# Performance work log

Hardware: AMD Instinct MI355X
Metric: run time of the kernel (lower is better)

The kernel has to match this reference:

```python
import jax, jax.numpy as jnp
import numpy as np

L = 18                      # tree depth, N = 2**L - 1 nodes (complete binary tree)
N = 2**L - 1               # 262143
D = 128                     # embedding dim
V = 100000                  # vocab size of the single data type
E = 8                       # edge_count


def setup_inputs() -> dict:
    key = jax.random.key(0)
    ks = jax.random.split(key, 8)
    data = jax.random.randint(ks[0], (N,), 0, V)
    edges = jax.random.randint(ks[1], (N,), 0, E)
    data_vecs = jax.random.normal(ks[2], (V, D), dtype=jnp.float32) * 0.1
    # torch uses torch.rand (U[0,1)); scaled for numerical stability over 18 levels
    data_W = jax.random.uniform(ks[3], (D, D), dtype=jnp.float32) * 0.1
    data_b = jax.random.uniform(ks[4], (D,), dtype=jnp.float32) * 0.1
    edge_W = jax.random.uniform(ks[5], (E, D, D), dtype=jnp.float32) * (2.0 / D)
    edge_b = jax.random.uniform(ks[6], (E, D), dtype=jnp.float32) * 0.1
    score_W = jax.random.uniform(ks[7], (D, 1), dtype=jnp.float32)
    return {"data": data, "edges": edges, "data_vecs": data_vecs,
            "data_W": data_W, "data_b": data_b, "edge_W": edge_W,
            "edge_b": edge_b, "score_W": score_W}


def reference(data, edges, data_vecs, data_W, data_b, edge_W, edge_b, score_W):
    # per-node leaf term: addmm(data_bias, data_vecs[data], data_W)  -> [N, D]
    raw = data_vecs[data] @ data_W + data_b
    ret = raw    # value returned to the parent (leaves: unclamped)
    emb = raw    # stored embedding (internal nodes: pre-clamp h)
    # bottom-up over levels; level l occupies indices [2**l - 1, 2**(l+1) - 1)
    for l in reversed(range(L - 1)):
        p0, npar = 2**l - 1, 2**l
        c0, M = 2**(l + 1) - 1, 2**(l + 1)
        child_ret = ret[c0:c0 + M]              # [M, D], siblings adjacent
        eids = edges[c0:c0 + M]                 # [M]
        # edge-weighted child transform: child @ edge_W[e] + edge_b[e]
        contrib = edge_b[eids]
        for e in range(E):                      # small static edge loop
            contrib = contrib + jnp.where((eids == e)[:, None], child_ret, 0.0) @ edge_W[e]
        # sum the two children of each parent, then (leaf + children) / (nc + 1)
        contrib = contrib.reshape(npar, 2, D).sum(axis=1)
        h = (raw[p0:p0 + npar] + contrib) / 3.0
        emb = emb.at[p0:p0 + npar].set(h)
        ret = ret.at[p0:p0 + npar].set(jnp.maximum(h, 0.0))
    scores = (emb @ score_W)[:, 0]              # [N]
    return scores


if __name__ == "__main__":
    out = reference(**setup_inputs())
    print(out.shape, out.dtype)
```

## Files before the change

### kernel.cpp

```cpp
#include <hip/hip_runtime.h>

#define D 128
#define NLVL 17
#define TS 128
#define LVLPAD 1024
#define LDSTR 136
#define LEAF_BLKS 1032
#define CHUNK 2048
#define CNT_BLKS 128

typedef float  floatx4 __attribute__((ext_vector_type(4)));
typedef short  shortx8 __attribute__((ext_vector_type(8)));

__device__ __forceinline__ unsigned short f2bf(float f) {
    unsigned u = __float_as_uint(f);
    u += 0x7FFFu + ((u >> 16) & 1u);
    return (unsigned short)(u >> 16);
}
__device__ __forceinline__ float bf2f(unsigned short h) {
    return __uint_as_float(((unsigned)h) << 16);
}
__device__ __forceinline__ int lvl_base_dev(int l) { return ((2 << l) - 2) + LVLPAD * l; }

__global__ __launch_bounds__(256) void prep_kernel(
    const float* __restrict__ dW, const float* __restrict__ db,
    const float* __restrict__ eW, const float* __restrict__ eb,
    const float* __restrict__ sWs, const float* __restrict__ vecs,
    const int* __restrict__ edges,
    unsigned short* __restrict__ ewt, unsigned short* __restrict__ cwt,
    unsigned short* __restrict__ dwt, float* __restrict__ dcomp,
    float* __restrict__ sv, float* __restrict__ s0, int* __restrict__ ctr,
    int* __restrict__ gcnt128, int Nn,
    unsigned short* __restrict__ vbf, int n4)
{
    __shared__ float smem[8448];
    const int b = blockIdx.x, t = threadIdx.x;
    if (b < 32) {
        float* w_s = smem;
        float* cs  = smem + 4096;
        const int e = b >> 2, cc = b & 3;
        for (int i = t; i < D * 8; i += 256) {
            const int k = i >> 3, j4 = i & 7;
            ((float4*)w_s)[i] = ((const float4*)eW)[((size_t)e * D + k) * 32 + cc * 8 + j4];
        }
        __syncthreads();
        const int r2 = t >> 1, h = t & 1;
        float4 acc[4];
        #pragma unroll
        for (int m = 0; m < 4; m++) acc[m] = make_float4(0.f, 0.f, 0.f, 0.f);
        for (int k = 0; k < D; k++) {
            const float a = dW[(size_t)r2 * D + k];
            #pragma unroll
            for (int m = 0; m < 4; m++) {
                const float4 w4 = ((const float4*)w_s)[k * 8 + h * 4 + m];
                acc[m].x += a * w4.x; acc[m].y += a * w4.y; acc[m].z += a * w4.z; acc[m].w += a * w4.w;
            }
        }
        #pragma unroll
        for (int m = 0; m < 4; m++) {
            cs[r2 * 33 + h * 16 + m * 4 + 0] = acc[m].x;
            cs[r2 * 33 + h * 16 + m * 4 + 1] = acc[m].y;
            cs[r2 * 33 + h * 16 + m * 4 + 2] = acc[m].z;
            cs[r2 * 33 + h * 16 + m * 4 + 3] = acc[m].w;
        }
        __syncthreads();
        {
            const int nn = t >> 3, kseg = t & 7, k0 = kseg * 16;
            unsigned ow[8];
            #pragma unroll
            for (int i2 = 0; i2 < 8; i2++) {
                const unsigned short lo = f2bf(cs[(k0 + 2 * i2) * 33 + nn]);
                const unsigned short hi = f2bf(cs[(k0 + 2 * i2 + 1) * 33 + nn]);
                ow[i2] = (unsigned)lo | ((unsigned)hi << 16);
            }
            uint4* dstp = (uint4*)(cwt + (size_t)e * D * D + (size_t)(cc * 32 + nn) * D + k0);
            dstp[0] = make_uint4(ow[0], ow[1], ow[2], ow[3]);
            dstp[1] = make_uint4(ow[4], ow[5], ow[6], ow[7]);
        }
        if (t < 32) {
            float a2 = 0.f;
            for (int k = 0; k < D; k++) a2 += db[k] * w_s[k * 32 + t];
            dcomp[e * D + cc * 32 + t] = a2 + eb[e * D + cc * 32 + t];
        }
    } else if (b < 41) {
        float* lds = smem;
        const int bb = b - 32;
        const float* src = (bb < 8) ? (eW + (size_t)bb * D * D) : dW;
        unsigned short* dst = (bb < 8) ? (ewt + (size_t)bb * D * D) : dwt;
        for (int half = 0; half < 2; half++) {
            __syncthreads();
            for (int i = t; i < 64 * D / 4; i += 256) {
                float4 v = ((const float4*)src)[half * (64 * D / 4) + i];
                const int k = (i * 4) >> 7, n = (i * 4) & 127;
                lds[k * 129 + n]     = v.x;
                lds[k * 129 + n + 1] = v.y;
                lds[k * 129 + n + 2] = v.z;
                lds[k * 129 + n + 3] = v.w;
            }
            __syncthreads();
            const int n = t >> 1, hh = t & 1;
            for (int kk = 0; kk < 32; kk++) {
                const int k = hh * 32 + kk;
                dst[(size_t)n * D + half * 64 + k] = f2bf(lds[k * 129 + n]);
            }
        }
    } else if (b == 41) {
        float* red = smem;
        if (t < 32) ctr[t] = 0;
        if (t < D) {
            float acc = 0.f;
            for (int j = 0; j < D; j++) acc += dW[(size_t)t * D + j] * sWs[j];
            sv[t] = acc;
        }
        red[t] = (t < D) ? db[t] * sWs[t] : 0.f;
        __syncthreads();
        for (int s = 128; s > 0; s >>= 1) { if (t < s) red[t] += red[t + s]; __syncthreads(); }
        if (t == 0) s0[0] = red[0];
    } else if (b < 42 + CNT_BLKS) {
        int* lc = (int*)smem;
        if (t < 32) lc[t] = 0;
        __syncthreads();
        for (int c = 16383 + (b - 42) * 256 + t; c < Nn; c += CNT_BLKS * 256) {
            const int e = edges[c];
            const int p = (c - 1) >> 1;
            const int l = 31 - __clz(p + 1);
            atomicAdd(&lc[(l - 13) * 8 + e], 1);
        }
        __syncthreads();
        if (t < 32) gcnt128[(b - 42) * 32 + t] = lc[t];
    } else {
        for (int i = (b - 42 - CNT_BLKS) * 256 + t; i < n4; i += (gridDim.x - 42 - CNT_BLKS) * 256) {
            const float4 v = ((const float4*)vecs)[i];
            uint2 o;
            o.x = (unsigned)f2bf(v.x) | ((unsigned)f2bf(v.y) << 16);
            o.y = (unsigned)f2bf(v.z) | ((unsigned)f2bf(v.w) << 16);
            ((uint2*)vbf)[i] = o;
        }
    }
}

__global__ __launch_bounds__(256) void place_kernel(
    const int* __restrict__ edges, const int* __restrict__ gcnt128,
    int* __restrict__ gstart, int* __restrict__ glim,
    int* __restrict__ ctr, int* __restrict__ perm, int Nn)
{
    __shared__ unsigned char key_s[CHUNK];
    __shared__ int part[256];
    __shared__ int tot[32];
    __shared__ int lcnt[32], lbase[32];
    __shared__ int gs_s[4 * 9], gl_s[32];
    const int t = threadIdx.x;
    {
        const int k = t & 31, bs = t >> 5;
        int s = 0;
        for (int bb = bs; bb < CNT_BLKS; bb += 8) s += gcnt128[bb * 32 + k];
        part[t] = s;
    }
    if (t < 32) lcnt[t] = 0;
    __syncthreads();
    if (t < 32) {
        int tt = 0;
        #pragma unroll
        for (int i = 0; i < 8; i++) tt += part[t + 32 * i];
        tot[t] = tt;
    }
    __syncthreads();
    if (t == 0) {
        for (int li = 0; li < 4; li++) {
            int acc = 0;
            for (int e = 0; e < 8; e++) {
                gs_s[li * 9 + e] = acc;
                gl_s[li * 8 + e] = acc + tot[li * 8 + e];
                acc = (acc + tot[li * 8 + e] + (TS - 1)) & ~(TS - 1);
            }
            gs_s[li * 9 + 8] = acc;
        }
    }
    __syncthreads();
    if (blockIdx.x == 0 && t < 36) {
        gstart[13 * 9 + t] = gs_s[t];
        if (t < 32) glim[13 * 8 + t] = gl_s[t];
    }
    const int base = 16383 + blockIdx.x * CHUNK;
    for (int i = t; i < CHUNK; i += 256) {
        const int c = base + i;
        if (c < Nn) {
            const int e = edges[c];
            const int p = (c - 1) >> 1;
            const int l = 31 - __clz(p + 1);
            const int kk = (l - 13) * 8 + e;
            key_s[i] = (unsigned char)kk;
            atomicAdd(&lcnt[kk], 1);
        } else key_s[i] = 255;
    }
    __syncthreads();
    if (t < 32) {
        const int n = lcnt[t];
        lbase[t] = n ? atomicAdd(&ctr[t], n) : 0;
        lcnt[t] = 0;
    }
    __syncthreads();
    for (int i = t; i < CHUNK; i += 256) {
        const int c = base + i;
        if (c >= Nn) continue;
        const int kk = key_s[i];
        if (kk == 255) continue;
        const int off = atomicAdd(&lcnt[kk], 1);
        const int l = (kk >> 3) + 13, e = kk & 7;
        const int pos = gs_s[(l - 13) * 9 + e] + lbase[kk] + off;
        perm[lvl_base_dev(l) + pos] = c;
    }
}

__global__ __launch_bounds__(256, 4) void leaf_embed_kernel(
    unsigned short* __restrict__ X,
    const unsigned short* __restrict__ vbf,
    const int* __restrict__ data,
    const int* __restrict__ perm,
    const int* __restrict__ gstart9,
    const int* __restrict__ glim8,
    const unsigned short* __restrict__ cwt,
    const float* __restrict__ dcomp,
    const float* __restrict__ sv, const float* __restrict__ s0p,
    const unsigned short* __restrict__ dwt,
    const float* __restrict__ db,
    float* __restrict__ out,
    int NI, int lbase_leaf)
{
    __shared__ unsigned short a_s[TS * LDSTR];
    const int t = threadIdx.x;
    const bool is_leaf = (blockIdx.x < LEAF_BLKS);
    const int r = t >> 1, h = t & 1;

    int e = 0, c;
    const unsigned short* Wg;
    const float* bias;
    if (is_leaf) {
        const int ts = blockIdx.x * TS;
        if (ts >= gstart9[8]) return;
        #pragma unroll
        for (int j = 1; j < 8; j++) if (ts >= gstart9[j]) e = j;
        const int p = ts + r;
        c = (p < glim8[e]) ? perm[lbase_leaf + p] : -1;
        Wg = cwt + (size_t)e * D * D;
        bias = dcomp + (size_t)e * D;
    } else {
        const int node = (blockIdx.x - LEAF_BLKS) * TS + r;
        c = (node < NI) ? node : -1;
        Wg = dwt;
        bias = db;
    }

    {
        unsigned short* dst = a_s + r * LDSTR + h * 64;
        if (c >= 0) {
            const uint4* src = (const uint4*)(vbf + (size_t)data[c] * D + h * 64);
            if (is_leaf) {
                float sc = 0.f;
                #pragma unroll
                for (int j = 0; j < 8; j++) {
                    const uint4 v = src[j];
                    const unsigned* pv = (const unsigned*)&v;
                    #pragma unroll
                    for (int u = 0; u < 4; u++) {
                        const int n = h * 64 + j * 8 + u * 2;
                        sc += bf2f((unsigned short)pv[u]) * sv[n]
                            + bf2f((unsigned short)(pv[u] >> 16)) * sv[n + 1];
                    }
                    ((uint4*)dst)[j] = v;
                }
                sc += __shfl_xor(sc, 1, 64);
                if (h == 0) out[c] = sc + s0p[0];
            } else {
                #pragma unroll
                for (int j = 0; j < 8; j++) ((uint4*)dst)[j] = src[j];
            }
        } else {
            #pragma unroll
            for (int j = 0; j < 8; j++) ((uint4*)dst)[j] = make_uint4(0u, 0u, 0u, 0u);
        }
    }
    __syncthreads();

    const int lane = t & 63, wv = t >> 6;
    const int cq = lane & 15, q = lane >> 4;
    const floatx4 z4 = {0.f, 0.f, 0.f, 0.f};
    floatx4 acc[8][2];
    #pragma unroll
    for (int i = 0; i < 8; i++) { acc[i][0] = z4; acc[i][1] = z4; }
    #pragma unroll
    for (int ks = 0; ks < 4; ks++) {
        shortx8 bfr[2];
        #pragma unroll
        for (int nl = 0; nl < 2; nl++) {
            const int n = (wv * 2 + nl) * 16 + cq;
            bfr[nl] = *(const shortx8*)(Wg + (size_t)n * D + ks * 32 + q * 8);
        }
        #pragma unroll
        for (int mt = 0; mt < 8; mt++) {
            const shortx8 af = *(const shortx8*)(a_s + (mt * 16 + cq) * LDSTR + ks * 32 + q * 8);
            acc[mt][0] = __builtin_amdgcn_mfma_f32_16x16x32_bf16(af, bfr[0], acc[mt][0], 0, 0, 0);
            acc[mt][1] = __builtin_amdgcn_mfma_f32_16x16x32_bf16(af, bfr[1], acc[mt][1], 0, 0, 0);
        }
    }
    __syncthreads();
    #pragma unroll
    for (int nl = 0; nl < 2; nl++) {
        const int n = (wv * 2 + nl) * 16 + cq;
        const float bn = bias[n];
        #pragma unroll
        for (int mt = 0; mt < 8; mt++) {
            #pragma unroll
            for (int rg = 0; rg < 4; rg++) {
                const int m = mt * 16 + q * 4 + rg;
                a_s[m * LDSTR + n] = f2bf(acc[mt][nl][rg] + bn);
            }
        }
    }
    __syncthreads();
    if (c >= 0) {
        uint4* dst = (uint4*)(X + (size_t)c * D + h * 64);
        const uint4* srcl = (const uint4*)(a_s + r * LDSTR + h * 64);
        #pragma unroll
        for (int j = 0; j < 8; j++) dst[j] = srcl[j];
    }
}

__global__ __launch_bounds__(256, 4) void tree_gemm_kernel(
    unsigned short* __restrict__ X,
    const int* __restrict__ perm,
    const int* __restrict__ gstart9,
    const int* __restrict__ glim8,
    const unsigned short* __restrict__ ewt,
    const float* __restrict__ eb,
    const float* __restrict__ svec,
    float* __restrict__ out,
    int lbase)
{
    __shared__ unsigned short a_s[TS * LDSTR];
    const int t = threadIdx.x;
    const int ts = blockIdx.x * TS;
    if (ts >= gstart9[8]) return;
    int e = 0;
    #pragma unroll
    for (int j = 1; j < 8; j++) if (ts >= gstart9[j]) e = j;
    const int r = t >> 1, h = t & 1;
    const int p = ts + r;
    const int c = (p < glim8[e]) ? perm[lbase + p] : -1;
    const unsigned short* Wg = ewt + (size_t)e * D * D;

    {
        unsigned short* dst = a_s + r * LDSTR + h * 64;
        if (c >= 0) {
            const uint4* xr = (const uint4*)(X + (size_t)c * D + h * 64);
            const uint4* ya = (const uint4*)(X + (size_t)(2 * c + 1) * D + h * 64);
            const uint4* yb = (const uint4*)(X + (size_t)(2 * c + 2) * D + h * 64);
            const float inv3 = 1.0f / 3.0f;
            float sc = 0.f;
            #pragma unroll
            for (int j = 0; j < 8; j++) {
                uint4 ra = xr[j], rb = ya[j], rc = yb[j];
                const unsigned* pa = (const unsigned*)&ra;
                const unsigned* pb = (const unsigned*)&rb;
                const unsigned* pc = (const unsigned*)&rc;
                unsigned ou[4];
                #pragma unroll
                for (int u = 0; u < 4; u++) {
                    const float h0 = (bf2f((unsigned short)pa[u]) + bf2f((unsigned short)pb[u])
                                    + bf2f((unsigned short)pc[u])) * inv3;
                    const float h1 = (bf2f((unsigned short)(pa[u] >> 16)) + bf2f((unsigned short)(pb[u] >> 16))
                                    + bf2f((unsigned short)(pc[u] >> 16))) * inv3;
                    const int n = h * 64 + j * 8 + u * 2;
                    sc += h0 * svec[n] + h1 * svec[n + 1];
                    unsigned short q0 = f2bf(h0), q1 = f2bf(h1);
                    q0 = (q0 & 0x8000u) ? 0 : q0;
                    q1 = (q1 & 0x8000u) ? 0 : q1;
                    ou[u] = (unsigned)q0 | ((unsigned)q1 << 16);
                }
                ((uint4*)dst)[j] = make_uint4(ou[0], ou[1], ou[2], ou[3]);
            }
            sc += __shfl_xor(sc, 1, 64);
            if (h == 0) out[c] = sc;
        } else {
            #pragma unroll
            for (int j = 0; j < 8; j++) ((uint4*)dst)[j] = make_uint4(0u, 0u, 0u, 0u);
        }
    }
    __syncthreads();
    const int lane = t & 63, wv = t >> 6;
    const int cq = lane & 15, q = lane >> 4;
    const floatx4 z4 = {0.f, 0.f, 0.f, 0.f};
    floatx4 acc[8][2];
    #pragma unroll
    for (int i = 0; i < 8; i++) { acc[i][0] = z4; acc[i][1] = z4; }
    #pragma unroll
    for (int ks = 0; ks < 4; ks++) {
        shortx8 bfr[2];
        #pragma unroll
        for (int nl = 0; nl < 2; nl++) {
            const int n = (wv * 2 + nl) * 16 + cq;
            bfr[nl] = *(const shortx8*)(Wg + (size_t)n * D + ks * 32 + q * 8);
        }
        #pragma unroll
        for (int mt = 0; mt < 8; mt++) {
            const shortx8 af = *(const shortx8*)(a_s + (mt * 16 + cq) * LDSTR + ks * 32 + q * 8);
            acc[mt][0] = __builtin_amdgcn_mfma_f32_16x16x32_bf16(af, bfr[0], acc[mt][0], 0, 0, 0);
            acc[mt][1] = __builtin_amdgcn_mfma_f32_16x16x32_bf16(af, bfr[1], acc[mt][1], 0, 0, 0);
        }
    }
    __syncthreads();
    #pragma unroll
    for (int nl = 0; nl < 2; nl++) {
        const int n = (wv * 2 + nl) * 16 + cq;
        const float bn = eb[(size_t)e * D + n];
        #pragma unroll
        for (int mt = 0; mt < 8; mt++) {
            #pragma unroll
            for (int rg = 0; rg < 4; rg++) {
                const int m = mt * 16 + q * 4 + rg;
                a_s[m * LDSTR + n] = f2bf(acc[mt][nl][rg] + bn);
            }
        }
    }
    __syncthreads();
    if (c >= 0) {
        uint4* dst = (uint4*)(X + (size_t)c * D + h * 64);
        const uint4* srcl = (const uint4*)(a_s + r * LDSTR + h * 64);
        #pragma unroll
        for (int j = 0; j < 8; j++) dst[j] = srcl[j];
    }
}

__global__ __launch_bounds__(256) void sub_kernel(
    unsigned short* __restrict__ X,
    const float* __restrict__ eW,
    const float* __restrict__ eb,
    const int* __restrict__ edges,
    const float* __restrict__ sW,
    float* __restrict__ out,
    int rbase, int nlev)
{
    __shared__ __align__(16) float xbuf[4][D];
    const int t = threadIdx.x, wv = t >> 6, lane = t & 63;
    const int u = rbase + blockIdx.x;
    const int j2 = lane * 2;
    const float inv3 = 1.0f / 3.0f;

    for (int lev = nlev - 1; lev >= 0; lev--) {
        const int first = ((u + 1) << lev) - 1;
        const int cnt = 1 << lev;
        for (int i = wv; i < cnt; i += 4) {
            const int n = first + i;
            const unsigned ra = *(const unsigned*)(X + (size_t)n * D + j2);
            const unsigned rb = *(const unsigned*)(X + (size_t)(2 * n + 1) * D + j2);
            const unsigned rc = *(const unsigned*)(X + (size_t)(2 * n + 2) * D + j2);
            const float h0 = (bf2f((unsigned short)ra) + bf2f((unsigned short)rb)
                            + bf2f((unsigned short)rc)) * inv3;
            const float h1 = (bf2f((unsigned short)(ra >> 16)) + bf2f((unsigned short)(rb >> 16))
                            + bf2f((unsigned short)(rc >> 16))) * inv3;
            float sc = h0 * sW[j2] + h1 * sW[j2 + 1];
            #pragma unroll
            for (int o = 32; o > 0; o >>= 1) sc += __shfl_xor(sc, o, 64);
            if (lane == 0) out[n] = sc;
            if (n == 0) continue;
            float2 x2 = make_float2(fmaxf(h0, 0.f), fmaxf(h1, 0.f));
            *(float2*)(xbuf[wv] + j2) = x2;
            const int e = edges[n];
            const float* W = eW + (size_t)e * D * D;
            float y0 = 0.f, y1 = 0.f;
            #pragma unroll 8
            for (int k4 = 0; k4 < 32; k4++) {
                const float4 xk = *(const float4*)(xbuf[wv] + k4 * 4);
                const float2 w0 = *(const float2*)(W + (size_t)(k4 * 4 + 0) * D + j2);
                const float2 w1 = *(const float2*)(W + (size_t)(k4 * 4 + 1) * D + j2);
                const float2 w2 = *(const float2*)(W + (size_t)(k4 * 4 + 2) * D + j2);
                const float2 w3 = *(const float2*)(W + (size_t)(k4 * 4 + 3) * D + j2);
                y0 += xk.x * w0.x + xk.y * w1.x + xk.z * w2.x + xk.w * w3.x;
                y1 += xk.x * w0.y + xk.y * w1.y + xk.z * w2.y + xk.w * w3.y;
            }
            y0 += eb[e * D + j2];
            y1 += eb[e * D + j2 + 1];
            const unsigned o = (unsigned)f2bf(y0) | ((unsigned)f2bf(y1) << 16);
            *(unsigned*)(X + (size_t)n * D + j2) = o;
        }
        __syncthreads();
    }
}

extern "C" void kernel_launch(void* const* d_in, const int* in_sizes, int n_in,
                              void* d_out, int out_size, void* d_ws, size_t ws_size,
                              hipStream_t stream) {
    const int*   data      = (const int*)d_in[0];
    const int*   edges     = (const int*)d_in[1];
    const float* data_vecs = (const float*)d_in[2];
    const float* data_W    = (const float*)d_in[3];
    const float* data_b    = (const float*)d_in[4];
    const float* edge_W    = (const float*)d_in[5];
    const float* edge_b    = (const float*)d_in[6];
    const float* score_W   = (const float*)d_in[7];
    float* out = (float*)d_out;

    const int Nn = in_sizes[0];
    const int NI = Nn >> 1;
    const int VD = in_sizes[2];
    const int PERM_TOTAL = (Nn - 1) + LVLPAD * NLVL;

    char* w = (char*)d_ws;
    size_t off = 0;
    unsigned short* X = (unsigned short*)(w + off); off += (size_t)Nn * D * 2;
    int* perm = (int*)(w + off);  off += (size_t)PERM_TOTAL * 4;
    off = (off + 255) & ~(size_t)255;
    int* gstart  = (int*)(w + off); off += NLVL * 9 * 4;
    int* glim    = (int*)(w + off); off += NLVL * 8 * 4;
    int* gcnt128 = (int*)(w + off); off += CNT_BLKS * 32 * 4;
    int* ctr     = (int*)(w + off); off += 32 * 4;
    off = (off + 255) & ~(size_t)255;
    float* dcomp = (float*)(w + off); off += 8 * D * 4;
    float* sv    = (float*)(w + off); off += D * 4;
    float* s0    = (float*)(w + off); off += 256;
    off = (off + 255) & ~(size_t)255;
    unsigned short* ewt = (unsigned short*)(w + off); off += (size_t)8 * D * D * 2;
    unsigned short* cwt = (unsigned short*)(w + off); off += (size_t)8 * D * D * 2;
    unsigned short* dwt = (unsigned short*)(w + off); off += (size_t)D * D * 2;
    off = (off + 255) & ~(size_t)255;
    unsigned short* vbf = (unsigned short*)(w + off); off += (size_t)VD * 2;

    prep_kernel<<<42 + CNT_BLKS + 1024, 256, 0, stream>>>(
        data_W, data_b, edge_W, edge_b, score_W, data_vecs, edges,
        ewt, cwt, dwt, dcomp, sv, s0, ctr, gcnt128, Nn, vbf, VD / 4);

    const int place_blks = (Nn - 16383 + CHUNK - 1) / CHUNK;
    place_kernel<<<place_blks, 256, 0, stream>>>(edges, gcnt128, gstart, glim, ctr, perm, Nn);

    {
        const int embed_blks = (NI + TS - 1) / TS;
        const int lbase_leaf = ((2 << 16) - 2) + LVLPAD * 16;
        leaf_embed_kernel<<<LEAF_BLKS + embed_blks, 256, 0, stream>>>(
            X, vbf, data, perm, gstart + 16 * 9, glim + 16 * 8,
            cwt, dcomp, sv, s0, dwt, data_b, out, NI, lbase_leaf);
    }

    for (int l = 15; l >= 13; l--) {
        const int M = 2 << l;
        const int lbase = ((2 << l) - 2) + LVLPAD * l;
        tree_gemm_kernel<<<M / TS + 8, 256, 0, stream>>>(
            X, perm, gstart + l * 9, glim + l * 8, ewt, edge_b, score_W, out, lbase);
    }

    sub_kernel<<<2048, 256, 0, stream>>>(X, edge_W, edge_b, edges, score_W, out, 2047, 3);
    sub_kernel<<<128, 256, 0, stream>>>(X, edge_W, edge_b, edges, score_W, out, 127, 4);
    sub_kernel<<<8, 256, 0, stream>>>(X, edge_W, edge_b, edges, score_W, out, 7, 4);
    sub_kernel<<<1, 256, 0, stream>>>(X, edge_W, edge_b, edges, score_W, out, 0, 3);
}
```

Before: 332.3 us.

## Assign one wavefront per subtree in top-level tree kernels with bf16 edge weights

Restructures the small top-of-tree kernels so that each wavefront owns a whole subtree and walks its levels without block-wide barriers. The last two tiny launches are merged into a single 512-thread kernel. Edge weights are pre-converted to bf16 in the prep kernel to halve weight traffic, and the GEMV is reorganized so each half-wave handles alternate k rows, combined with a cross-half shuffle. This cuts launch count and synchronisation, at the cost of less parallelism per subtree, an explicit waitcnt per node to order the dependent global reads, and bf16 rounding of the weights.

```diff
diff --git a/kernel.cpp b/kernel.cpp
--- a/kernel.cpp
+++ b/kernel.cpp
@@ -20,6 +20,9 @@
 __device__ __forceinline__ float bf2f(unsigned short h) {
     return __uint_as_float(((unsigned)h) << 16);
 }
+__device__ __forceinline__ float bf2f_hi(unsigned u) {
+    return __uint_as_float(u & 0xFFFF0000u);
+}
 __device__ __forceinline__ int lvl_base_dev(int l) { return ((2 << l) - 2) + LVLPAD * l; }
 
 __global__ __launch_bounds__(256) void prep_kernel(
@@ -28,7 +31,8 @@
     const float* __restrict__ sWs, const float* __restrict__ vecs,
     const int* __restrict__ edges,
     unsigned short* __restrict__ ewt, unsigned short* __restrict__ cwt,
-    unsigned short* __restrict__ dwt, float* __restrict__ dcomp,
+    unsigned short* __restrict__ dwt, unsigned short* __restrict__ ebk,
+    float* __restrict__ dcomp,
     float* __restrict__ sv, float* __restrict__ s0, int* __restrict__ ctr,
     int* __restrict__ gcnt128, int Nn,
     unsigned short* __restrict__ vbf, int n4)
@@ -128,8 +132,17 @@
         }
         __syncthreads();
         if (t < 32) gcnt128[(b - 42) * 32 + t] = lc[t];
+    } else if (b < 42 + CNT_BLKS + 32) {
+        const int n4e = 8 * D * D / 4;
+        for (int i = (b - 42 - CNT_BLKS) * 256 + t; i < n4e; i += 32 * 256) {
+            const float4 v = ((const float4*)eW)[i];
+            uint2 o;
+            o.x = (unsigned)f2bf(v.x) | ((unsigned)f2bf(v.y) << 16);
+            o.y = (unsigned)f2bf(v.z) | ((unsigned)f2bf(v.w) << 16);
+            ((uint2*)ebk)[i] = o;
+        }
     } else {
-        for (int i = (b - 42 - CNT_BLKS) * 256 + t; i < n4; i += (gridDim.x - 42 - CNT_BLKS) * 256) {
+        for (int i = (b - 42 - CNT_BLKS - 32) * 256 + t; i < n4; i += (gridDim.x - 42 - CNT_BLKS - 32) * 256) {
             const float4 v = ((const float4*)vecs)[i];
             uint2 o;
             o.x = (unsigned)f2bf(v.x) | ((unsigned)f2bf(v.y) << 16);
@@ -431,9 +444,62 @@
     }
 }
 
-__global__ __launch_bounds__(256) void sub_kernel(
+__device__ __forceinline__ void node_step(
     unsigned short* __restrict__ X,
-    const float* __restrict__ eW,
+    const unsigned short* __restrict__ ebk,
+    const float* __restrict__ eb,
+    const int* __restrict__ edges,
+    const float* __restrict__ sW,
+    float* __restrict__ out,
+    float* __restrict__ xb,
+    int n, int lane)
+{
+    __builtin_amdgcn_s_waitcnt(0);
+    const int j2 = lane * 2;
+    const unsigned ra = *(const unsigned*)(X + (size_t)n * D + j2);
+    const unsigned rb = *(const unsigned*)(X + (size_t)(2 * n + 1) * D + j2);
+    const unsigned rc = *(const unsigned*)(X + (size_t)(2 * n + 2) * D + j2);
+    const float inv3 = 1.0f / 3.0f;
+    const float h0 = (bf2f((unsigned short)ra) + bf2f((unsigned short)rb)
+                    + bf2f((unsigned short)rc)) * inv3;
+    const float h1 = (bf2f_hi(ra) + bf2f_hi(rb) + bf2f_hi(rc)) * inv3;
+    float sc = h0 * sW[j2] + h1 * sW[j2 + 1];
+    #pragma unroll
+    for (int o = 32; o > 0; o >>= 1) sc += __shfl_xor(sc, o, 64);
+    if (lane == 0) out[n] = sc;
+    if (n == 0) return;
+    *(float2*)(xb + j2) = make_float2(fmaxf(h0, 0.f), fmaxf(h1, 0.f));
+    const int e = edges[n];
+    const unsigned short* W = ebk + (size_t)e * D * D;
+    const int p = lane >> 5;
+    const int c4 = (lane & 31) * 4;
+    float y0 = 0.f, y1 = 0.f, y2 = 0.f, y3 = 0.f;
+    #pragma unroll 8
+    for (int k2 = 0; k2 < 64; k2++) {
+        const int k = 2 * k2 + p;
+        const float xk = xb[k];
+        const uint2 w = *(const uint2*)(W + (size_t)k * D + c4);
+        y0 += xk * bf2f((unsigned short)w.x);
+        y1 += xk * bf2f_hi(w.x);
+        y2 += xk * bf2f((unsigned short)w.y);
+        y3 += xk * bf2f_hi(w.y);
+    }
+    y0 += __shfl_xor(y0, 32, 64);
+    y1 += __shfl_xor(y1, 32, 64);
+    y2 += __shfl_xor(y2, 32, 64);
+    y3 += __shfl_xor(y3, 32, 64);
+    if (lane < 32) {
+        const float4 b4 = *(const float4*)(eb + e * D + c4);
+        uint2 o;
+        o.x = (unsigned)f2bf(y0 + b4.x) | ((unsigned)f2bf(y1 + b4.y) << 16);
+        o.y = (unsigned)f2bf(y2 + b4.z) | ((unsigned)f2bf(y3 + b4.w) << 16);
+        *(uint2*)(X + (size_t)n * D + c4) = o;
+    }
+}
+
+__global__ __launch_bounds__(256) void subw_kernel(
+    unsigned short* __restrict__ X,
+    const unsigned short* __restrict__ ebk,
     const float* __restrict__ eb,
     const int* __restrict__ edges,
     const float* __restrict__ sW,
@@ -442,48 +508,42 @@
 {
     __shared__ __align__(16) float xbuf[4][D];
     const int t = threadIdx.x, wv = t >> 6, lane = t & 63;
-    const int u = rbase + blockIdx.x;
-    const int j2 = lane * 2;
-    const float inv3 = 1.0f / 3.0f;
-
+    const int u = rbase + blockIdx.x * 4 + wv;
     for (int lev = nlev - 1; lev >= 0; lev--) {
         const int first = ((u + 1) << lev) - 1;
         const int cnt = 1 << lev;
-        for (int i = wv; i < cnt; i += 4) {
-            const int n = first + i;
-            const unsigned ra = *(const unsigned*)(X + (size_t)n * D + j2);
-            const unsigned rb = *(const unsigned*)(X + (size_t)(2 * n + 1) * D + j2);
-            const unsigned rc = *(const unsigned*)(X + (size_t)(2 * n + 2) * D + j2);
-            const float h0 = (bf2f((unsigned short)ra) + bf2f((unsigned short)rb)
-                            + bf2f((unsigned short)rc)) * inv3;
-            const float h1 = (bf2f((unsigned short)(ra >> 16)) + bf2f((unsigned short)(rb >> 16))
-                            + bf2f((unsigned short)(rc >> 16))) * inv3;
-            float sc = h0 * sW[j2] + h1 * sW[j2 + 1];
-            #pragma unroll
-            for (int o = 32; o > 0; o >>= 1) sc += __shfl_xor(sc, o, 64);
-            if (lane == 0) out[n] = sc;
-            if (n == 0) continue;
-            float2 x2 = make_float2(fmaxf(h0, 0.f), fmaxf(h1, 0.f));
-            *(float2*)(xbuf[wv] + j2) = x2;
-            const int e = edges[n];
-            const float* W = eW + (size_t)e * D * D;
-            float y0 = 0.f, y1 = 0.f;
-            #pragma unroll 8
-            for (int k4 = 0; k4 < 32; k4++) {
-                const float4 xk = *(const float4*)(xbuf[wv] + k4 * 4);
-                const float2 w0 = *(const float2*)(W + (size_t)(k4 * 4 + 0) * D + j2);
-                const float2 w1 = *(const float2*)(W + (size_t)(k4 * 4 + 1) * D + j2);
-                const float2 w2 = *(const float2*)(W + (size_t)(k4 * 4 + 2) * D + j2);
-                const float2 w3 = *(const float2*)(W + (size_t)(k4 * 4 + 3) * D + j2);
-                y0 += xk.x * w0.x + xk.y * w1.x + xk.z * w2.x + xk.w * w3.x;
-                y1 += xk.x * w0.y + xk.y * w1.y + xk.z * w2.y + xk.w * w3.y;
-            }
-            y0 += eb[e * D + j2];
-            y1 += eb[e * D + j2 + 1];
-            const unsigned o = (unsigned)f2bf(y0) | ((unsigned)f2bf(y1) << 16);
-            *(unsigned*)(X + (size_t)n * D + j2) = o;
-        }
-        __syncthreads();
+        for (int i = 0; i < cnt; i++)
+            node_step(X, ebk, eb, edges, sW, out, xbuf[wv], first + i, lane);
+    }
+}
+
+__global__ __launch_bounds__(512) void subtop_kernel(
+    unsigned short* __restrict__ X,
+    const unsigned short* __restrict__ ebk,
+    const float* __restrict__ eb,
+    const int* __restrict__ edges,
+    const float* __restrict__ sW,
+    float* __restrict__ out)
+{
+    __shared__ __align__(16) float xbuf[8][D];
+    const int t = threadIdx.x, wv = t >> 6, lane = t & 63;
+    {
+        const int u = 7 + wv;
+        for (int lev = 3; lev >= 0; lev--) {
+            const int first = ((u + 1) << lev) - 1;
+            const int cnt = 1 << lev;
+            for (int i = 0; i < cnt; i++)
+                node_step(X, ebk, eb, edges, sW, out, xbuf[wv], first + i, lane);
+        }
+    }
+    __syncthreads();
+    if (wv == 0) {
+        for (int lev = 2; lev >= 0; lev--) {
+            const int first = (1 << lev) - 1;
+            const int cnt = 1 << lev;
+            for (int i = 0; i < cnt; i++)
+                node_step(X, ebk, eb, edges, sW, out, xbuf[0], first + i, lane);
+        }
     }
 }
 
@@ -522,12 +582,13 @@
     unsigned short* ewt = (unsigned short*)(w + off); off += (size_t)8 * D * D * 2;
     unsigned short* cwt = (unsigned short*)(w + off); off += (size_t)8 * D * D * 2;
     unsigned short* dwt = (unsigned short*)(w + off); off += (size_t)D * D * 2;
+    unsigned short* ebk = (unsigned short*)(w + off); off += (size_t)8 * D * D * 2;
     off = (off + 255) & ~(size_t)255;
     unsigned short* vbf = (unsigned short*)(w + off); off += (size_t)VD * 2;
 
-    prep_kernel<<<42 + CNT_BLKS + 1024, 256, 0, stream>>>(
+    prep_kernel<<<42 + CNT_BLKS + 32 + 1024, 256, 0, stream>>>(
         data_W, data_b, edge_W, edge_b, score_W, data_vecs, edges,
-        ewt, cwt, dwt, dcomp, sv, s0, ctr, gcnt128, Nn, vbf, VD / 4);
+        ewt, cwt, dwt, ebk, dcomp, sv, s0, ctr, gcnt128, Nn, vbf, VD / 4);
 
     const int place_blks = (Nn - 16383 + CHUNK - 1) / CHUNK;
     place_kernel<<<place_blks, 256, 0, stream>>>(edges, gcnt128, gstart, glim, ctr, perm, Nn);
@@ -547,8 +608,7 @@
             X, perm, gstart + l * 9, glim + l * 8, ewt, edge_b, score_W, out, lbase);
     }
 
-    sub_kernel<<<2048, 256, 0, stream>>>(X, edge_W, edge_b, edges, score_W, out, 2047, 3);
-    sub_kernel<<<128, 256, 0, stream>>>(X, edge_W, edge_b, edges, score_W, out, 127, 4);
-    sub_kernel<<<8, 256, 0, stream>>>(X, edge_W, edge_b, edges, score_W, out, 7, 4);
-    sub_kernel<<<1, 256, 0, stream>>>(X, edge_W, edge_b, edges, score_W, out, 0, 3);
-}
+    subw_kernel<<<512, 256, 0, stream>>>(X, ebk, edge_b, edges, score_W, out, 2047, 3);
+    subw_kernel<<<32, 256, 0, stream>>>(X, ebk, edge_b, edges, score_W, out, 127, 4);
+    subtop_kernel<<<1, 512, 0, stream>>>(X, ebk, edge_b, edges, score_W, out);
+}
```

After: 389.6 us. 17.3% more time.
